# Optimization experiments

Hardware: AMD Instinct MI355X
Metric: run time of the kernel (lower is better)

The kernel has to match this reference:

```python
import jax, jax.numpy as jnp
import numpy as np

RADIUS_IN = 0.05
RADIUS_OUT = 0.2
NSAMPLE = 32


def setup_inputs() -> dict:
    key = jax.random.key(0)
    k1, k2, k3 = jax.random.split(key, 3)
    B, N, M, C = 2, 16384, 2048, 64
    xyz = jax.random.uniform(k1, (B, N, 3), dtype=jnp.float32)
    new_xyz = jax.random.uniform(k2, (B, M, 3), dtype=jnp.float32)
    features = jax.random.normal(k3, (B, C, N), dtype=jnp.float32)
    return {"xyz": xyz, "new_xyz": new_xyz, "features": features}


def _ball_query_dilated(xyz, new_xyz, r_in, r_out, nsample):
    # xyz: (B,N,3), new_xyz: (B,M,3)
    d2 = jnp.sum((new_xyz[:, :, None, :] - xyz[:, None, :, :]) ** 2, axis=-1)  # (B,M,N)
    mask = (d2 >= r_in * r_in) & (d2 < r_out * r_out)  # dilated shell
    B, M, N = mask.shape
    rank = jnp.cumsum(mask, axis=-1) - 1  # order of each match along N
    cnt = jnp.minimum(jnp.sum(mask, axis=-1), nsample).astype(jnp.int32)  # (B,M)
    # scatter the j-th point index into slot `rank` (overflow slots dumped into pad)
    pos = jnp.where(mask & (rank < nsample), rank, nsample)
    b = jnp.arange(B)[:, None, None]
    m = jnp.arange(M)[None, :, None]
    j = jnp.broadcast_to(jnp.arange(N, dtype=jnp.int32)[None, None, :], (B, M, N))
    idx = jnp.zeros((B, M, nsample + 1), jnp.int32).at[b, m, pos].set(j)[..., :nsample]
    # CUDA kernel fills unused slots with the FIRST matched index (0 if no match)
    slot = jnp.arange(nsample)[None, None, :]
    idx = jnp.where(slot < cnt[..., None], idx, idx[..., :1])
    return cnt, idx


def _group(features, idx):
    # features: (B,C,N), idx: (B,M,S) -> (B,C,M,S)
    B, C, N = features.shape
    _, M, S = idx.shape
    flat = idx.reshape(B, 1, M * S)
    return jnp.take_along_axis(features, flat, axis=2).reshape(B, C, M, S)


def reference(xyz, new_xyz, features):
    idx_cnt, idx = _ball_query_dilated(xyz, new_xyz, RADIUS_IN, RADIUS_OUT, NSAMPLE)
    xyz_t = jnp.transpose(xyz, (0, 2, 1))            # (B,3,N)
    grouped_xyz = _group(xyz_t, idx)                 # (B,3,M,S)
    grouped_xyz = grouped_xyz - jnp.transpose(new_xyz, (0, 2, 1))[..., None]
    grouped_features = _group(features, idx)         # (B,C,M,S)
    new_features = jnp.concatenate([grouped_xyz, grouped_features], axis=1)
    return idx_cnt, new_features
```

## Files before the change

### kernel.cpp

```cpp
#include <hip/hip_runtime.h>
#include <cstdint>

#define BB 2
#define NN 16384
#define MM 2048
#define CC 64
#define SS 32

__device__ __forceinline__ float dist2(float qx, float qy, float qz,
                                       float px, float py, float pz) {
    float dx = __fsub_rn(qx, px), dy = __fsub_rn(qy, py), dz = __fsub_rn(qz, pz);
    return __fadd_rn(__fadd_rn(__fmul_rn(dx, dx), __fmul_rn(dy, dy)), __fmul_rn(dz, dz));
}

__global__ void prep_xyz4(const float* __restrict__ xyz, float4* __restrict__ xyz4) {
    int i = blockIdx.x * 256 + threadIdx.x;
    if (i < BB * NN) {
        xyz4[i] = make_float4(xyz[3 * i], xyz[3 * i + 1], xyz[3 * i + 2], 0.f);
    }
}

__global__ void transpose_feat(const float* __restrict__ f, float* __restrict__ ft) {
    __shared__ float tile[32][33];
    int b = blockIdx.z, n0 = blockIdx.x * 32, c0 = blockIdx.y * 32;
    int tx = threadIdx.x, ty = threadIdx.y;
#pragma unroll
    for (int k = 0; k < 32; k += 8)
        tile[ty + k][tx] = f[((size_t)(b * CC + c0 + ty + k)) * NN + n0 + tx];
    __syncthreads();
#pragma unroll
    for (int k = 0; k < 32; k += 8)
        ft[((size_t)(b * NN + n0 + ty + k)) * CC + c0 + tx] = tile[tx][ty + k];
}

template <bool FAST>
__global__ __launch_bounds__(64) void query_group(
    const float* __restrict__ xyz, const float* __restrict__ new_xyz,
    const float* __restrict__ features, const float* __restrict__ feat_t,
    const float4* __restrict__ xyz4, float* __restrict__ out) {
    constexpr float R_IN2 = 0.05f * 0.05f;
    constexpr float R_OUT2 = 0.2f * 0.2f;
    __shared__ int idxS[SS];
    __shared__ float fbuf[SS][CC + 4];

    int lane = threadIdx.x;
    int bm = blockIdx.x;
    int b = bm >> 11;
    int m = bm & 2047;

    float qx = new_xyz[(size_t)bm * 3 + 0];
    float qy = new_xyz[(size_t)bm * 3 + 1];
    float qz = new_xyz[(size_t)bm * 3 + 2];

    if (lane == 0) idxS[0] = 0;

    unsigned long long below = (1ull << lane) - 1ull;
    int cnt = 0;
    for (int j0 = 0; j0 < NN; j0 += 256) {
        float px[4], py[4], pz[4];
        if (FAST) {
            const float4* base = xyz4 + b * NN + j0 + lane;
#pragma unroll
            for (int u = 0; u < 4; ++u) {
                float4 p = base[u * 64];
                px[u] = p.x; py[u] = p.y; pz[u] = p.z;
            }
        } else {
            const float* pp = xyz + ((size_t)(b * NN + j0 + lane)) * 3;
#pragma unroll
            for (int u = 0; u < 4; ++u) {
                px[u] = pp[u * 192 + 0];
                py[u] = pp[u * 192 + 1];
                pz[u] = pp[u * 192 + 2];
            }
        }
#pragma unroll
        for (int u = 0; u < 4; ++u) {
            float d2 = dist2(qx, qy, qz, px[u], py[u], pz[u]);
            bool inshell = (d2 >= R_IN2) && (d2 < R_OUT2);
            unsigned long long mk = __ballot(inshell);
            if (inshell) {
                int r = cnt + __popcll(mk & below);
                if (r < SS) idxS[r] = j0 + u * 64 + lane;
            }
            cnt += __popcll(mk);
        }
        if (cnt >= SS) break;
    }
    if (cnt > SS) cnt = SS;
    if (lane == 0) out[bm] = (float)cnt;
    __syncthreads();

    float* gout = out + BB * MM;

    if (FAST) {
        int s4 = lane >> 4, c4 = lane & 15;
#pragma unroll
        for (int it = 0; it < 8; ++it) {
            int sl = it * 4 + s4;
            int j = (sl < cnt) ? idxS[sl] : idxS[0];
            const float4* src = (const float4*)(feat_t + ((size_t)b * NN + j) * CC);
            float4 v = src[c4];
            *((float4*)&fbuf[sl][c4 * 4]) = v;
        }
        __syncthreads();
    }

    int s = lane & 31, half = lane >> 5;
    int j = (s < cnt) ? idxS[s] : idxS[0];

    float px, py, pz;
    if (FAST) {
        float4 p = xyz4[b * NN + j];
        px = p.x; py = p.y; pz = p.z;
    } else {
        const float* pp = xyz + ((size_t)(b * NN) + j) * 3;
        px = pp[0]; py = pp[1]; pz = pp[2];
    }

    {
        float v01 = half ? __fsub_rn(py, qy) : __fsub_rn(px, qx);
        gout[((size_t)(b * 67 + half) * MM + m) * SS + s] = v01;
        if (half == 0) {
            gout[((size_t)(b * 67 + 2) * MM + m) * SS + s] = __fsub_rn(pz, qz);
        }
    }

#pragma unroll
    for (int k = 0; k < 32; ++k) {
        int ch = 2 * k + half;
        float v = FAST ? fbuf[s][ch]
                       : features[((size_t)(b * CC + ch)) * NN + j];
        gout[((size_t)(b * 67 + 3 + ch) * MM + m) * SS + s] = v;
    }
}

extern "C" void kernel_launch(void* const* d_in, const int* in_sizes, int n_in,
                              void* d_out, int out_size, void* d_ws, size_t ws_size,
                              hipStream_t stream) {
    const float* xyz = (const float*)d_in[0];
    const float* new_xyz = (const float*)d_in[1];
    const float* features = (const float*)d_in[2];
    float* out = (float*)d_out;

    const size_t featT_bytes = (size_t)BB * NN * CC * 4;
    const size_t xyz4_bytes = (size_t)BB * NN * 16;
    bool fast = ws_size >= featT_bytes + xyz4_bytes;

    if (fast) {
        float* feat_t = (float*)d_ws;
        float4* xyz4 = (float4*)((char*)d_ws + featT_bytes);
        prep_xyz4<<<(BB * NN + 255) / 256, 256, 0, stream>>>(xyz, xyz4);
        dim3 tg(NN / 32, CC / 32, BB);
        transpose_feat<<<tg, dim3(32, 8), 0, stream>>>(features, feat_t);
        query_group<true><<<BB * MM, 64, 0, stream>>>(xyz, new_xyz, features, feat_t, xyz4, out);
    } else {
        query_group<false><<<BB * MM, 64, 0, stream>>>(xyz, new_xyz, features, nullptr, nullptr, out);
    }
}
```

Before: 93.18 us.

## Fuse prep kernels into one launch and pack four queries per block

```diff
diff --git a/kernel.cpp b/kernel.cpp
--- a/kernel.cpp
+++ b/kernel.cpp
@@ -6,6 +6,7 @@
 #define MM 2048
 #define CC 64
 #define SS 32
+#define WPB 4
 
 __device__ __forceinline__ float dist2(float qx, float qy, float qz,
                                        float px, float py, float pz) {
@@ -13,38 +14,44 @@
     return __fadd_rn(__fadd_rn(__fmul_rn(dx, dx), __fmul_rn(dy, dy)), __fmul_rn(dz, dz));
 }
 
-__global__ void prep_xyz4(const float* __restrict__ xyz, float4* __restrict__ xyz4) {
-    int i = blockIdx.x * 256 + threadIdx.x;
-    if (i < BB * NN) {
-        xyz4[i] = make_float4(xyz[3 * i], xyz[3 * i + 1], xyz[3 * i + 2], 0.f);
+__global__ __launch_bounds__(256) void prep_fused(
+    const float* __restrict__ xyz, const float* __restrict__ f,
+    float* __restrict__ ft, float4* __restrict__ xyz4) {
+    int bid = blockIdx.x;
+    if (bid < 2048) {
+        __shared__ float tile[32][33];
+        int n0 = (bid & 511) * 32;
+        int c0 = ((bid >> 9) & 1) * 32;
+        int b = bid >> 10;
+        int tx = threadIdx.x & 31, ty = threadIdx.x >> 5;
+#pragma unroll
+        for (int k = 0; k < 32; k += 8)
+            tile[ty + k][tx] = f[((size_t)(b * CC + c0 + ty + k)) * NN + n0 + tx];
+        __syncthreads();
+#pragma unroll
+        for (int k = 0; k < 32; k += 8)
+            ft[((size_t)(b * NN + n0 + ty + k)) * CC + c0 + tx] = tile[tx][ty + k];
+    } else {
+        int i = (bid - 2048) * 256 + threadIdx.x;
+        if (i < BB * NN) {
+            xyz4[i] = make_float4(xyz[3 * i], xyz[3 * i + 1], xyz[3 * i + 2], 0.f);
+        }
     }
 }
 
-__global__ void transpose_feat(const float* __restrict__ f, float* __restrict__ ft) {
-    __shared__ float tile[32][33];
-    int b = blockIdx.z, n0 = blockIdx.x * 32, c0 = blockIdx.y * 32;
-    int tx = threadIdx.x, ty = threadIdx.y;
-#pragma unroll
-    for (int k = 0; k < 32; k += 8)
-        tile[ty + k][tx] = f[((size_t)(b * CC + c0 + ty + k)) * NN + n0 + tx];
-    __syncthreads();
-#pragma unroll
-    for (int k = 0; k < 32; k += 8)
-        ft[((size_t)(b * NN + n0 + ty + k)) * CC + c0 + tx] = tile[tx][ty + k];
-}
-
 template <bool FAST>
-__global__ __launch_bounds__(64) void query_group(
+__global__ __launch_bounds__(64 * WPB) void query_group(
     const float* __restrict__ xyz, const float* __restrict__ new_xyz,
     const float* __restrict__ features, const float* __restrict__ feat_t,
     const float4* __restrict__ xyz4, float* __restrict__ out) {
     constexpr float R_IN2 = 0.05f * 0.05f;
     constexpr float R_OUT2 = 0.2f * 0.2f;
-    __shared__ int idxS[SS];
-    __shared__ float fbuf[SS][CC + 4];
+    __shared__ int idxS[WPB][SS];
+    __shared__ float fbuf[WPB][SS][CC + 4];
 
-    int lane = threadIdx.x;
-    int bm = blockIdx.x;
+    int lane = threadIdx.x & 63;
+    int w = threadIdx.x >> 6;
+    int bm = blockIdx.x * WPB + w;
     int b = bm >> 11;
     int m = bm & 2047;
 
@@ -52,7 +59,7 @@
     float qy = new_xyz[(size_t)bm * 3 + 1];
     float qz = new_xyz[(size_t)bm * 3 + 2];
 
-    if (lane == 0) idxS[0] = 0;
+    if (lane == 0) idxS[w][0] = 0;
 
     unsigned long long below = (1ull << lane) - 1ull;
     int cnt = 0;
@@ -81,7 +88,7 @@
             unsigned long long mk = __ballot(inshell);
             if (inshell) {
                 int r = cnt + __popcll(mk & below);
-                if (r < SS) idxS[r] = j0 + u * 64 + lane;
+                if (r < SS) idxS[w][r] = j0 + u * 64 + lane;
             }
             cnt += __popcll(mk);
         }
@@ -89,7 +96,6 @@
     }
     if (cnt > SS) cnt = SS;
     if (lane == 0) out[bm] = (float)cnt;
-    __syncthreads();
 
     float* gout = out + BB * MM;
 
@@ -98,16 +104,15 @@
 #pragma unroll
         for (int it = 0; it < 8; ++it) {
             int sl = it * 4 + s4;
-            int j = (sl < cnt) ? idxS[sl] : idxS[0];
+            int j = (sl < cnt) ? idxS[w][sl] : idxS[w][0];
             const float4* src = (const float4*)(feat_t + ((size_t)b * NN + j) * CC);
             float4 v = src[c4];
-            *((float4*)&fbuf[sl][c4 * 4]) = v;
+            *((float4*)&fbuf[w][sl][c4 * 4]) = v;
         }
-        __syncthreads();
     }
 
     int s = lane & 31, half = lane >> 5;
-    int j = (s < cnt) ? idxS[s] : idxS[0];
+    int j = (s < cnt) ? idxS[w][s] : idxS[w][0];
 
     float px, py, pz;
     if (FAST) {
@@ -129,7 +134,7 @@
 #pragma unroll
     for (int k = 0; k < 32; ++k) {
         int ch = 2 * k + half;
-        float v = FAST ? fbuf[s][ch]
+        float v = FAST ? fbuf[w][s][ch]
                        : features[((size_t)(b * CC + ch)) * NN + j];
         gout[((size_t)(b * 67 + 3 + ch) * MM + m) * SS + s] = v;
     }
@@ -150,11 +155,9 @@
     if (fast) {
         float* feat_t = (float*)d_ws;
         float4* xyz4 = (float4*)((char*)d_ws + featT_bytes);
-        prep_xyz4<<<(BB * NN + 255) / 256, 256, 0, stream>>>(xyz, xyz4);
-        dim3 tg(NN / 32, CC / 32, BB);
-        transpose_feat<<<tg, dim3(32, 8), 0, stream>>>(features, feat_t);
-        query_group<true><<<BB * MM, 64, 0, stream>>>(xyz, new_xyz, features, feat_t, xyz4, out);
+        prep_fused<<<2048 + 128, 256, 0, stream>>>(xyz, features, feat_t, xyz4);
+        query_group<true><<<BB * MM / WPB, 64 * WPB, 0, stream>>>(xyz, new_xyz, features, feat_t, xyz4, out);
     } else {
-        query_group<false><<<BB * MM, 64, 0, stream>>>(xyz, new_xyz, features, nullptr, nullptr, out);
+        query_group<false><<<BB * MM / WPB, 64 * WPB, 0, stream>>>(xyz, new_xyz, features, nullptr, nullptr, out);
     }
 }
```

Result: no change. 92.23 us (-1.0%).
